# Optimization experiments

Hardware: AMD Instinct MI355X
Metric: run time of the kernel (lower is better)

## Reference

```python
import jax, jax.numpy as jnp
import numpy as np

B, D, H = 8192, 1024, 1024

def setup_inputs() -> dict:
    key = jax.random.key(0)
    ks = jax.random.split(key, 7)
    s_x = 1.0 / np.sqrt(D)
    s_h = 1.0 / np.sqrt(H)
    return {
        "e_t": jax.random.normal(ks[0], (B, D), jnp.float32),
        "h_prev": jax.random.normal(ks[1], (B, H), jnp.float32),
        "c_prev": jax.random.normal(ks[2], (B, H), jnp.float32),
        # gates concatenated in order (f, i, o, c), each block of size H
        "W_x": jax.random.uniform(ks[3], (4 * H, D), jnp.float32, -s_x, s_x),
        "b_x": jax.random.uniform(ks[4], (4 * H,), jnp.float32, -s_x, s_x),
        "W_h": jax.random.uniform(ks[5], (4 * H, H), jnp.float32, -s_h, s_h),
        "b_h": jax.random.uniform(ks[6], (4 * H,), jnp.float32, -s_h, s_h),
        "b_extra": jnp.zeros((4 * H,), jnp.float32),  # the b_f/b_i/b_o/b_c Parameters
    }

def reference(e_t, h_prev, c_prev, W_x, b_x, W_h, b_h, b_extra):
    # two fused GEMMs: [B,D]@[D,4H] and [B,H]@[H,4H]
    z = (jnp.einsum('bd,gd->bg', e_t, W_x)
         + jnp.einsum('bh,gh->bg', h_prev, W_h)
         + b_x + b_h + b_extra)  # [B, 4H]
    zf, zi, zo, zc = jnp.split(z, 4, axis=-1)
    g_t = jax.nn.sigmoid(zf)   # forget gate
    p_t = jax.nn.sigmoid(zi)   # input gate
    q_t = jax.nn.sigmoid(zo)   # output gate
    m_t_hat = jnp.tanh(zc)     # candidate cell
    c_t = g_t * c_prev + p_t * m_t_hat
    h_t = q_t * jnp.tanh(c_t)
    return (h_t, c_t)
```

## Files before the change

kernel.cpp:

```cpp
#include <hip/hip_runtime.h>
#include <stdint.h>

#define B_ROWS 8192
#define DH     1024
#define KTOT   2048
#define NTOT   4096

typedef __attribute__((ext_vector_type(8))) __bf16 bf16x8;
typedef __attribute__((ext_vector_type(4))) float  f32x4;

__device__ __forceinline__ unsigned short f2bf(float f) {
    unsigned int u = __float_as_uint(f);
    u += 0x7FFFu + ((u >> 16) & 1u);
    return (unsigned short)(u >> 16);
}

__device__ __forceinline__ float fast_sigmoid(float x) {
    return 1.0f / (1.0f + __expf(-x));
}
__device__ __forceinline__ float fast_tanh(float x) {
    float e = __expf(fminf(-2.0f * x, 80.0f));
    return (1.0f - e) / (1.0f + e);
}

#define NBLK_A (B_ROWS)
#define NBLK_W (NTOT)
#define NBLK_BIAS (NTOT / 256)

__global__ __launch_bounds__(256) void pack_all(const float* __restrict__ e_t,
                                                const float* __restrict__ h_prev,
                                                const float* __restrict__ W_x,
                                                const float* __restrict__ W_h,
                                                const float* __restrict__ b_x,
                                                const float* __restrict__ b_h,
                                                const float* __restrict__ b_e,
                                                unsigned short* __restrict__ A_cat,
                                                unsigned short* __restrict__ W_cat,
                                                float* __restrict__ bias) {
    const int blk = blockIdx.x;
    const int t   = threadIdx.x;
    if (blk < NBLK_A + NBLK_W) {
        const float* src0;
        unsigned short* dst;
        int row;
        if (blk < NBLK_A) {
            row = blk;
            dst = A_cat + (size_t)row * KTOT;
            int c8 = t << 3;
            src0 = (c8 < DH) ? (e_t + (size_t)row * DH + c8)
                             : (h_prev + (size_t)row * DH + (c8 - DH));
        } else {
            row = blk - NBLK_A;
            int gate = (row >> 4) & 3;
            int h    = (row >> 6) * 16 + (row & 15);
            int srow = gate * DH + h;
            dst = W_cat + (size_t)row * KTOT;
            int c8 = t << 3;
            src0 = (c8 < DH) ? (W_x + (size_t)srow * DH + c8)
                             : (W_h + (size_t)srow * DH + (c8 - DH));
        }
        float4 f0 = ((const float4*)src0)[0];
        float4 f1 = ((const float4*)src0)[1];
        uint4 o;
        o.x = (unsigned)f2bf(f0.x) | ((unsigned)f2bf(f0.y) << 16);
        o.y = (unsigned)f2bf(f0.z) | ((unsigned)f2bf(f0.w) << 16);
        o.z = (unsigned)f2bf(f1.x) | ((unsigned)f2bf(f1.y) << 16);
        o.w = (unsigned)f2bf(f1.z) | ((unsigned)f2bf(f1.w) << 16);
        *(uint4*)(dst + t * 8) = o;
    } else {
        int gp = (blk - NBLK_A - NBLK_W) * 256 + t;
        int gate = (gp >> 4) & 3;
        int h    = (gp >> 6) * 16 + (gp & 15);
        int g    = gate * DH + h;
        bias[gp] = b_x[g] + b_h[g] + b_e[g];
    }
}


#define GLL(srcp, dstp) \
    __builtin_amdgcn_global_load_lds( \
        (const __attribute__((address_space(1))) void*)(srcp), \
        (__attribute__((address_space(3))) void*)(dstp), 16, 0, 0)

#define STAGE_HALF(g, buf, h, kt) do { \
    GLL((g) + ((size_t)((h) * 128)      * KTOT) + (size_t)(kt) * 64, (buf) + (((h) * 128)      + w8) * 128); \
    GLL((g) + ((size_t)((h) * 128 + 64) * KTOT) + (size_t)(kt) * 64, (buf) + (((h) * 128 + 64) + w8) * 128); \
} while (0)

#define SB() __builtin_amdgcn_sched_barrier(0)

#define PHASE_SYNC() do { \
    SB(); \
    __builtin_amdgcn_s_barrier(); \
    asm volatile("s_waitcnt lgkmcnt(0)" ::: "memory"); \
    SB(); \
} while (0)

#define PHASE_CLOSE() do { \
    SB(); \
    __builtin_amdgcn_s_barrier(); \
    SB(); \
} while (0)

template <int MODE>
__device__ __forceinline__ void do_tile(
    int kt,
    unsigned char* As_cur, unsigned char* As_next, unsigned char* Bs_cur,
    const unsigned short* __restrict__ gA, const unsigned short* __restrict__ gB,
    int w8, int rowA, int rowB, int xg0, int xg1,
    f32x4 (&acc)[8][4])
{
    bf16x8 al[4], b[4];

#pragma unroll
    for (int mi = 0; mi < 4; ++mi)
        al[mi] = *(const bf16x8*)(As_cur + rowA + mi * 2048 + xg0);
#pragma unroll
    for (int ni = 0; ni < 4; ++ni)
        b[ni] = *(const bf16x8*)(Bs_cur + rowB + ni * 2048 + xg0);
    if constexpr (MODE >= 1) STAGE_HALF(gA, As_next, 0, kt + 1);
    PHASE_SYNC();
    __builtin_amdgcn_s_setprio(1);
#pragma unroll
    for (int mi = 0; mi < 4; ++mi)
#pragma unroll
        for (int ni = 0; ni < 4; ++ni)
            acc[mi][ni] = __builtin_amdgcn_mfma_f32_16x16x32_bf16(al[mi], b[ni], acc[mi][ni], 0, 0, 0);
    __builtin_amdgcn_s_setprio(0);
    PHASE_CLOSE();

    bf16x8 ah[4];
#pragma unroll
    for (int mi = 0; mi < 4; ++mi)
        ah[mi] = *(const bf16x8*)(As_cur + rowA + (4 + mi) * 2048 + xg0);
    if constexpr (MODE >= 1) STAGE_HALF(gA, As_next, 1, kt + 1);
    PHASE_SYNC();
    __builtin_amdgcn_s_setprio(1);
#pragma unroll
    for (int mi = 0; mi < 4; ++mi)
#pragma unroll
        for (int ni = 0; ni < 4; ++ni)
            acc[4 + mi][ni] = __builtin_amdgcn_mfma_f32_16x16x32_bf16(ah[mi], b[ni], acc[4 + mi][ni], 0, 0, 0);
    __builtin_amdgcn_s_setprio(0);
    PHASE_CLOSE();

#pragma unroll
    for (int mi = 0; mi < 4; ++mi)
        al[mi] = *(const bf16x8*)(As_cur + rowA + mi * 2048 + xg1);
#pragma unroll
    for (int ni = 0; ni < 4; ++ni)
        b[ni] = *(const bf16x8*)(Bs_cur + rowB + ni * 2048 + xg1);
    PHASE_SYNC();
    __builtin_amdgcn_s_setprio(1);
#pragma unroll
    for (int mi = 0; mi < 4; ++mi)
#pragma unroll
        for (int ni = 0; ni < 4; ++ni)
            acc[mi][ni] = __builtin_amdgcn_mfma_f32_16x16x32_bf16(al[mi], b[ni], acc[mi][ni], 0, 0, 0);
    __builtin_amdgcn_s_setprio(0);
    PHASE_CLOSE();

#pragma unroll
    for (int mi = 0; mi < 4; ++mi)
        ah[mi] = *(const bf16x8*)(As_cur + rowA + (4 + mi) * 2048 + xg1);
    if constexpr (MODE == 2) {
        STAGE_HALF(gB, Bs_cur, 0, kt + 2);
        STAGE_HALF(gB, Bs_cur, 1, kt + 2);
    }
    PHASE_SYNC();
    __builtin_amdgcn_s_setprio(1);
#pragma unroll
    for (int mi = 0; mi < 4; ++mi)
#pragma unroll
        for (int ni = 0; ni < 4; ++ni)
            acc[4 + mi][ni] = __builtin_amdgcn_mfma_f32_16x16x32_bf16(ah[mi], b[ni], acc[4 + mi][ni], 0, 0, 0);
    __builtin_amdgcn_s_setprio(0);
    SB();
    if constexpr (MODE == 2) {
        asm volatile("s_waitcnt vmcnt(4)" ::: "memory");
        SB();
    } else if constexpr (MODE == 1) {
        asm volatile("s_waitcnt vmcnt(0)" ::: "memory");
        SB();
    }
    __builtin_amdgcn_s_barrier();
    SB();
}

__global__ __launch_bounds__(512, 2) void lstm_gemm(
    const unsigned short* __restrict__ A,
    const unsigned short* __restrict__ Wc,
    const float* __restrict__ bias,
    const float* __restrict__ c_prev,
    float* __restrict__ h_out,
    float* __restrict__ c_out)
{
    __shared__ __align__(16) unsigned char lds[131072];

    const int tid = threadIdx.x;
    const int w   = tid >> 6;
    const int l   = tid & 63;
    const int wm  = w >> 2, wn = w & 3;
    const int m0  = blockIdx.y * 256;
    const int n0  = blockIdx.x * 256;
    const int w8  = w * 8;

    f32x4 acc[8][4];
#pragma unroll
    for (int i = 0; i < 8; ++i)
#pragma unroll
        for (int j = 0; j < 4; ++j) acc[i][j] = {0.f, 0.f, 0.f, 0.f};

    const int srow = w8 + (l >> 3);
    const int scol = ((l & 7) ^ ((l >> 3) & 7)) * 8;
    const unsigned short* gA = A  + (size_t)(m0 + srow) * KTOT + scol;
    const unsigned short* gB = Wc + (size_t)(n0 + srow) * KTOT + scol;

    unsigned char* As0 = lds;
    unsigned char* As1 = lds + 32768;
    unsigned char* Bs0 = lds + 65536;
    unsigned char* Bs1 = lds + 98304;

    const int lane15 = l & 15;
    const int quad   = l >> 4;
    const int rowA = (wm * 128 + lane15) * 128;
    const int rowB = (wn * 64  + lane15) * 128;
    const int xg0  = ((0 + quad) ^ (lane15 & 7)) * 16;
    const int xg1  = ((4 + quad) ^ (lane15 & 7)) * 16;

    STAGE_HALF(gA, As0, 0, 0);
    STAGE_HALF(gA, As0, 1, 0);
    STAGE_HALF(gB, Bs0, 0, 0);
    STAGE_HALF(gB, Bs0, 1, 0);
    STAGE_HALF(gB, Bs1, 0, 1);
    STAGE_HALF(gB, Bs1, 1, 1);
    SB();
    asm volatile("s_waitcnt vmcnt(4)" ::: "memory");
    SB();
    __builtin_amdgcn_s_barrier();
    SB();

#pragma unroll 1
    for (int kt2 = 0; kt2 < 15; ++kt2) {
        do_tile<2>(2 * kt2,     As0, As1, Bs0, gA, gB, w8, rowA, rowB, xg0, xg1, acc);
        do_tile<2>(2 * kt2 + 1, As1, As0, Bs1, gA, gB, w8, rowA, rowB, xg0, xg1, acc);
    }
    do_tile<1>(30, As0, As1, Bs0, gA, gB, w8, rowA, rowB, xg0, xg1, acc);
    do_tile<0>(31, As1, As0, Bs1, gA, gB, w8, rowA, rowB, xg0, xg1, acc);

    float biasv[4];
#pragma unroll
    for (int nj = 0; nj < 4; ++nj)
        biasv[nj] = bias[n0 + wn * 64 + nj * 16 + lane15];

    const int hcol = ((n0 + wn * 64) >> 6) * 16 + lane15;

#pragma unroll
    for (int mi = 0; mi < 8; ++mi) {
        const int mbase = m0 + wm * 128 + mi * 16 + quad * 4;
        f32x4 zf4 = acc[mi][0];
        f32x4 zi4 = acc[mi][1];
        f32x4 zo4 = acc[mi][2];
        f32x4 zc4 = acc[mi][3];
#pragma unroll
        for (int r = 0; r < 4; ++r) {
            float zf = zf4[r] + biasv[0];
            float zi = zi4[r] + biasv[1];
            float zo = zo4[r] + biasv[2];
            float zc = zc4[r] + biasv[3];

            float gf = fast_sigmoid(zf);
            float gi = fast_sigmoid(zi);
            float go = fast_sigmoid(zo);
            float mh = fast_tanh(zc);

            const size_t off = (size_t)(mbase + r) * DH + hcol;
            float cp = c_prev[off];
            float ct = gf * cp + gi * mh;
            float ht = go * fast_tanh(ct);
            h_out[off] = ht;
            c_out[off] = ct;
        }
    }
}

extern "C" void kernel_launch(void* const* d_in, const int* in_sizes, int n_in,
                              void* d_out, int out_size, void* d_ws, size_t ws_size,
                              hipStream_t stream) {
    const float* e_t     = (const float*)d_in[0];
    const float* h_prev  = (const float*)d_in[1];
    const float* c_prev  = (const float*)d_in[2];
    const float* W_x     = (const float*)d_in[3];
    const float* b_x     = (const float*)d_in[4];
    const float* W_h     = (const float*)d_in[5];
    const float* b_h     = (const float*)d_in[6];
    const float* b_extra = (const float*)d_in[7];

    float* h_out = (float*)d_out;
    float* c_out = h_out + (size_t)B_ROWS * DH;

    unsigned short* A_cat = (unsigned short*)d_ws;
    unsigned short* W_cat = (unsigned short*)((char*)d_ws + (size_t)B_ROWS * KTOT * 2);
    float*          bias  = (float*)((char*)d_ws + (size_t)B_ROWS * KTOT * 2 + (size_t)NTOT * KTOT * 2);

    pack_all<<<NBLK_A + NBLK_W + NBLK_BIAS, 256, 0, stream>>>(
        e_t, h_prev, W_x, W_h, b_x, b_h, b_extra, A_cat, W_cat, bias);
    lstm_gemm<<<dim3(NTOT / 256, B_ROWS / 256), 512, 0, stream>>>(
        A_cat, W_cat, bias, c_prev, h_out, c_out);
}
```

Measured before the change: 303.9 us.

## Replace per-phase barriers with counted lgkmcnt waits and early LDS prefetch

Drops the two s_barriers per MFMA phase in the GEMM tile loop. All LDS fragment reads for the tile are issued up front, using more registers, and each MFMA phase waits only on its own reads through graded lgkmcnt counts. The A-next global-to-LDS staging is issued all at once. A single barrier is kept before restaging B into the current buffer, plus one at the end. This cuts synchronization stalls and increases overlap, but raises register pressure, and barrier removal in MODE 0 could risk LDS hazards.

```diff
diff --git a/kernel.cpp b/kernel.cpp
--- a/kernel.cpp
+++ b/kernel.cpp
@@ -89,18 +89,7 @@
 
 #define SB() __builtin_amdgcn_sched_barrier(0)
 
-#define PHASE_SYNC() do { \
-    SB(); \
-    __builtin_amdgcn_s_barrier(); \
-    asm volatile("s_waitcnt lgkmcnt(0)" ::: "memory"); \
-    SB(); \
-} while (0)
-
-#define PHASE_CLOSE() do { \
-    SB(); \
-    __builtin_amdgcn_s_barrier(); \
-    SB(); \
-} while (0)
+#define WAIT_LGKM(n) do { SB(); asm volatile("s_waitcnt lgkmcnt(" #n ")" ::: "memory"); SB(); } while (0)
 
 template <int MODE>
 __device__ __forceinline__ void do_tile(
@@ -110,81 +99,90 @@
     int w8, int rowA, int rowB, int xg0, int xg1,
     f32x4 (&acc)[8][4])
 {
-    bf16x8 al[4], b[4];
-
-#pragma unroll
-    for (int mi = 0; mi < 4; ++mi)
-        al[mi] = *(const bf16x8*)(As_cur + rowA + mi * 2048 + xg0);
+    bf16x8 al0[4], ah[4], al1[4], b0[4], b1[4];
+
+#pragma unroll
+    for (int mi = 0; mi < 4; ++mi)
+        al0[mi] = *(const bf16x8*)(As_cur + rowA + mi * 2048 + xg0);
 #pragma unroll
     for (int ni = 0; ni < 4; ++ni)
-        b[ni] = *(const bf16x8*)(Bs_cur + rowB + ni * 2048 + xg0);
-    if constexpr (MODE >= 1) STAGE_HALF(gA, As_next, 0, kt + 1);
-    PHASE_SYNC();
+        b0[ni] = *(const bf16x8*)(Bs_cur + rowB + ni * 2048 + xg0);
+#pragma unroll
+    for (int mi = 0; mi < 4; ++mi)
+        ah[mi] = *(const bf16x8*)(As_cur + rowA + (4 + mi) * 2048 + xg0);
+    if constexpr (MODE >= 1) {
+        STAGE_HALF(gA, As_next, 0, kt + 1);
+        STAGE_HALF(gA, As_next, 1, kt + 1);
+    }
+#pragma unroll
+    for (int mi = 0; mi < 4; ++mi)
+        al1[mi] = *(const bf16x8*)(As_cur + rowA + mi * 2048 + xg1);
+#pragma unroll
+    for (int ni = 0; ni < 4; ++ni)
+        b1[ni] = *(const bf16x8*)(Bs_cur + rowB + ni * 2048 + xg1);
+
+    WAIT_LGKM(12);
     __builtin_amdgcn_s_setprio(1);
 #pragma unroll
     for (int mi = 0; mi < 4; ++mi)
 #pragma unroll
         for (int ni = 0; ni < 4; ++ni)
-            acc[mi][ni] = __builtin_amdgcn_mfma_f32_16x16x32_bf16(al[mi], b[ni], acc[mi][ni], 0, 0, 0);
+            acc[mi][ni] = __builtin_amdgcn_mfma_f32_16x16x32_bf16(al0[mi], b0[ni], acc[mi][ni], 0, 0, 0);
     __builtin_amdgcn_s_setprio(0);
-    PHASE_CLOSE();
-
-    bf16x8 ah[4];
-#pragma unroll
-    for (int mi = 0; mi < 4; ++mi)
-        ah[mi] = *(const bf16x8*)(As_cur + rowA + (4 + mi) * 2048 + xg0);
-    if constexpr (MODE >= 1) STAGE_HALF(gA, As_next, 1, kt + 1);
-    PHASE_SYNC();
+    SB();
+
+    WAIT_LGKM(8);
     __builtin_amdgcn_s_setprio(1);
 #pragma unroll
     for (int mi = 0; mi < 4; ++mi)
 #pragma unroll
         for (int ni = 0; ni < 4; ++ni)
-            acc[4 + mi][ni] = __builtin_amdgcn_mfma_f32_16x16x32_bf16(ah[mi], b[ni], acc[4 + mi][ni], 0, 0, 0);
+            acc[4 + mi][ni] = __builtin_amdgcn_mfma_f32_16x16x32_bf16(ah[mi], b0[ni], acc[4 + mi][ni], 0, 0, 0);
     __builtin_amdgcn_s_setprio(0);
-    PHASE_CLOSE();
-
-#pragma unroll
-    for (int mi = 0; mi < 4; ++mi)
-        al[mi] = *(const bf16x8*)(As_cur + rowA + mi * 2048 + xg1);
-#pragma unroll
-    for (int ni = 0; ni < 4; ++ni)
-        b[ni] = *(const bf16x8*)(Bs_cur + rowB + ni * 2048 + xg1);
-    PHASE_SYNC();
+    SB();
+
+#pragma unroll
+    for (int mi = 0; mi < 4; ++mi)
+        ah[mi] = *(const bf16x8*)(As_cur + rowA + (4 + mi) * 2048 + xg1);
+
+    WAIT_LGKM(4);
     __builtin_amdgcn_s_setprio(1);
 #pragma unroll
     for (int mi = 0; mi < 4; ++mi)
 #pragma unroll
         for (int ni = 0; ni < 4; ++ni)
-            acc[mi][ni] = __builtin_amdgcn_mfma_f32_16x16x32_bf16(al[mi], b[ni], acc[mi][ni], 0, 0, 0);
+            acc[mi][ni] = __builtin_amdgcn_mfma_f32_16x16x32_bf16(al1[mi], b1[ni], acc[mi][ni], 0, 0, 0);
     __builtin_amdgcn_s_setprio(0);
-    PHASE_CLOSE();
-
-#pragma unroll
-    for (int mi = 0; mi < 4; ++mi)
-        ah[mi] = *(const bf16x8*)(As_cur + rowA + (4 + mi) * 2048 + xg1);
+    SB();
+
+    __builtin_amdgcn_s_barrier();
+    SB();
     if constexpr (MODE == 2) {
         STAGE_HALF(gB, Bs_cur, 0, kt + 2);
         STAGE_HALF(gB, Bs_cur, 1, kt + 2);
     }
-    PHASE_SYNC();
+
+    WAIT_LGKM(0);
     __builtin_amdgcn_s_setprio(1);
 #pragma unroll
     for (int mi = 0; mi < 4; ++mi)
 #pragma unroll
         for (int ni = 0; ni < 4; ++ni)
-            acc[4 + mi][ni] = __builtin_amdgcn_mfma_f32_16x16x32_bf16(ah[mi], b[ni], acc[4 + mi][ni], 0, 0, 0);
+            acc[4 + mi][ni] = __builtin_amdgcn_mfma_f32_16x16x32_bf16(ah[mi], b1[ni], acc[4 + mi][ni], 0, 0, 0);
     __builtin_amdgcn_s_setprio(0);
     SB();
+
     if constexpr (MODE == 2) {
         asm volatile("s_waitcnt vmcnt(4)" ::: "memory");
+        SB();
+        __builtin_amdgcn_s_barrier();
         SB();
     } else if constexpr (MODE == 1) {
         asm volatile("s_waitcnt vmcnt(0)" ::: "memory");
         SB();
-    }
-    __builtin_amdgcn_s_barrier();
-    SB();
+        __builtin_amdgcn_s_barrier();
+        SB();
+    }
 }
 
 __global__ __launch_bounds__(512, 2) void lstm_gemm(
```

Result: no change. 300.0 us (-1.3%).
